# Kernel tuning notes

Measured on AMD Instinct MI355X. Metric: run time of the kernel, lower is better.

## Reference

```python
import jax, jax.numpy as jnp
import numpy as np

PAD_LABEL = 15
NUM_TAGS = 15


def setup_inputs() -> dict:
    key = jax.random.key(0)
    k1, k2, k3 = jax.random.split(key, 3)
    B, T, C = 4096, 512, NUM_TAGS
    logits = jax.random.normal(k1, (B, T, C), dtype=jnp.float32)
    y_true = jax.random.randint(k2, (B, T), 0, PAD_LABEL + 1, dtype=jnp.int32)
    # CRF transition matrix (learned param), glorot-ish scale
    transitions = jax.random.normal(k3, (C, C), dtype=jnp.float32) * 0.25
    return {"logits": logits, "y_true": y_true, "transitions": transitions}


def _log_norm(logits, transitions, mask):
    # logits: (B, T, C) float32, mask: (B, T) bool
    alpha0 = logits[:, 0, :]                       # (B, C)
    # scan over timesteps 1..T-1
    emits = jnp.swapaxes(logits[:, 1:, :], 0, 1)    # (T-1, B, C)
    masks = jnp.swapaxes(mask[:, 1:], 0, 1)         # (T-1, B)

    def step(alpha, inp):
        emit_t, mask_t = inp                        # (B, C), (B,)
        # scores[b, i, j] = alpha[b, i] + trans[i, j] + emit_t[b, j]
        scores = alpha[:, :, None] + transitions[None, :, :] + emit_t[:, None, :]
        new_alpha = jax.scipy.special.logsumexp(scores, axis=1)  # (B, C)
        alpha = jnp.where(mask_t[:, None], new_alpha, alpha)
        return alpha, None

    alpha, _ = jax.lax.scan(step, alpha0, (emits, masks))
    return jax.scipy.special.logsumexp(alpha, axis=1)  # (B,)


def _sequence_score(logits, transitions, labels, mask):
    mask_f = mask.astype(jnp.float32)
    safe_labels = jnp.where(mask, labels, 0)                    # (B, T)
    # emission scores along gold path
    em = jnp.take_along_axis(logits, safe_labels[:, :, None], axis=2)[:, :, 0]
    emission_score = jnp.sum(em * mask_f, axis=1)               # (B,)
    # transition scores between consecutive valid positions
    prev, curr = safe_labels[:, :-1], safe_labels[:, 1:]
    tmask_f = (mask[:, 1:] & mask[:, :-1]).astype(jnp.float32)
    trans_scores = transitions[prev, curr]                      # (B, T-1)
    transition_score = jnp.sum(trans_scores * tmask_f, axis=1)  # (B,)
    return emission_score + transition_score


def reference(logits, y_true, transitions):
    mask = y_true != PAD_LABEL                                  # (B, T) bool
    logZ = _log_norm(logits, transitions, mask)
    path_score = _sequence_score(logits, transitions, y_true, mask)
    nll = jnp.clip(logZ - path_score, 0.0, 1000000.0)
    return jnp.mean(nll)
```

## Files before the change

kernel.cpp:

```cpp
#include <hip/hip_runtime.h>
#include <hip/hip_bf16.h>

#define PAD 15
#define NTAGS 15
#define SEQ_T 512
#define SPB 8
#define LOG2E 1.4426950408889634f
#define LN2   0.6931471805599453f

__device__ __forceinline__ float max15(const float* A) {
  float m0 = fmaxf(fmaxf(A[0], A[1]), A[2]);
  float m1 = fmaxf(fmaxf(A[3], A[4]), A[5]);
  float m2 = fmaxf(fmaxf(A[6], A[7]), A[8]);
  float m3 = fmaxf(fmaxf(A[9], A[10]), A[11]);
  float m4 = fmaxf(fmaxf(A[12], A[13]), A[14]);
  return fmaxf(fmaxf(fmaxf(m0, m1), fmaxf(m2, m3)), m4);
}

__device__ __forceinline__ float dot15(const float* a, const float* b) {
  float d0 = a[0] * b[0], d1 = a[1] * b[1], d2 = a[2] * b[2];
  d0 = fmaf(a[3], b[3], d0);  d1 = fmaf(a[4], b[4], d1);  d2 = fmaf(a[5], b[5], d2);
  d0 = fmaf(a[6], b[6], d0);  d1 = fmaf(a[7], b[7], d1);  d2 = fmaf(a[8], b[8], d2);
  d0 = fmaf(a[9], b[9], d0);  d1 = fmaf(a[10], b[10], d1); d2 = fmaf(a[11], b[11], d2);
  d0 = fmaf(a[12], b[12], d0); d1 = fmaf(a[13], b[13], d1); d2 = fmaf(a[14], b[14], d2);
  return (d0 + d1) + d2;
}

__device__ __forceinline__ void bcast_read(const float4* slot4, float* E) {
  asm volatile("" ::: "memory");
  float4 u0 = slot4[0], u1 = slot4[1], u2 = slot4[2], u3 = slot4[3];
  E[0] = u0.x; E[1] = u0.y; E[2]  = u0.z; E[3]  = u0.w;
  E[4] = u1.x; E[5] = u1.y; E[6]  = u1.z; E[7]  = u1.w;
  E[8] = u2.x; E[9] = u2.y; E[10] = u2.z; E[11] = u2.w;
  E[12] = u3.x; E[13] = u3.y; E[14] = u3.z;
}

__global__ __launch_bounds__(256, 2)
void crf_fwdbwd(const float* __restrict__ logits, const int* __restrict__ yg,
                const float* __restrict__ trans, float* __restrict__ out)
{
  __shared__ float Tl[256];
  __shared__ int   yl[SPB * SEQ_T];
  __shared__ float bc[16][16];
  __shared__ float comb[SPB][32];
  __shared__ float blks[SPB];

  const int tid = threadIdx.x;

  Tl[tid] = (tid < NTAGS * NTAGS) ? trans[tid] : 0.0f;
  {
    const int4* src = (const int4*)(yg + (size_t)blockIdx.x * (SPB * SEQ_T));
    int4* dst = (int4*)yl;
    #pragma unroll
    for (int k = 0; k < (SPB * SEQ_T / 4) / 256; ++k)
      dst[tid + k * 256] = src[tid + k * 256];
  }
  __syncthreads();

  const int wave = tid >> 6;
  const int lane = tid & 63;
  const int j  = lane & 15;
  const int jj = (j < 15) ? j : 14;
  const int sLoc = (wave >> 1) * 4 + (lane >> 4);
  const bool isFwd = (wave & 1) == 0;
  const int seq = blockIdx.x * SPB + sLoc;
  float* slot = &bc[tid >> 4][0];
  const float4* slot4 = (const float4*)slot;
  const int* ys = &yl[sLoc * SEQ_T];
  const float* ebase = logits + (size_t)seq * (SEQ_T * NTAGS) + jj;

  float W[15];
  float pacc = 0.0f;

  if (isFwd) {
    #pragma unroll
    for (int i = 0; i < 15; ++i) W[i] = exp2f(Tl[i * 15 + jj] * LOG2E);

    float a0 = ebase[0];
    int yp = ys[0];
    pacc = (j == yp && yp != PAD) ? a0 : 0.0f;
    slot[j] = a0 * LOG2E;
    float A[15];
    bcast_read(slot4, A);
    float M = max15(A);
    float E[15];
    #pragma unroll
    for (int i = 0; i < 15; ++i) E[i] = exp2f(A[i] - M);
    float Eown = E[jj];

    float buf[8];
    #pragma unroll
    for (int k = 0; k < 8; ++k) buf[k] = ebase[(1 + k) * 15];

    for (int tb = 1; tb <= 241; tb += 8) {
      #pragma unroll
      for (int k = 0; k < 8; ++k) {
        const int t = tb + k;
        float emit = buf[k];
        int tn = t + 8; tn = (tn > 255) ? 255 : tn;
        buf[k] = ebase[tn * 15];
        int yc = ys[t];
        float p = exp2f(emit * LOG2E);
        float dot = dot15(E, W);
        float newE = dot * p;
        bool mk = (yc != PAD);
        float own = mk ? newE : Eown;
        float tv = Tl[yp * 15 + yc];
        float add = emit + ((yp != PAD) ? tv : 0.0f);
        pacc += (mk && (j == yc)) ? add : 0.0f;
        slot[j] = own;
        bcast_read(slot4, E);
        Eown = own;
        yp = yc;
        if (k == 7) {
          float m = max15(E);
          float rs = 1.0f / m;
          #pragma unroll
          for (int i = 0; i < 15; ++i) E[i] *= rs;
          Eown *= rs;
          M += log2f(m);
        }
      }
    }
    #pragma unroll
    for (int k = 0; k < 7; ++k) {
      const int t = 249 + k;
      float emit = buf[k];
      int yc = ys[t];
      float p = exp2f(emit * LOG2E);
      float dot = dot15(E, W);
      float newE = dot * p;
      bool mk = (yc != PAD);
      float own = mk ? newE : Eown;
      float tv = Tl[yp * 15 + yc];
      float add = emit + ((yp != PAD) ? tv : 0.0f);
      pacc += (mk && (j == yc)) ? add : 0.0f;
      slot[j] = own;
      bcast_read(slot4, E);
      Eown = own;
      yp = yc;
    }
    #pragma unroll
    for (int k = 1; k < 16; k <<= 1) pacc += __shfl_xor(pacc, k, 16);
    if (j < 15) comb[sLoc][j] = M + log2f(Eown);
    if (j == 0) comb[sLoc][30] = pacc;
  } else {
    #pragma unroll
    for (int i = 0; i < 15; ++i) W[i] = exp2f(Tl[jj * 15 + i] * LOG2E);

    float Eb = 1.0f, Mb = 0.0f;
    int yc = ys[511];
    float buf[8];
    #pragma unroll
    for (int k = 0; k < 8; ++k) buf[k] = ebase[(511 - k) * 15];

    float Q[15];
    for (int tb = 511; tb >= 271; tb -= 8) {
      #pragma unroll
      for (int k = 0; k < 8; ++k) {
        const int t = tb - k;
        float emit = buf[k];
        int tn = t - 8; tn = (tn < 256) ? 256 : tn;
        buf[k] = ebase[tn * 15];
        int yp2 = ys[t - 1];
        float p = exp2f(emit * LOG2E);
        float q = Eb * p;
        slot[j] = q;
        bcast_read(slot4, Q);
        float dot = dot15(W, Q);
        bool mk = (yc != PAD);
        Eb = mk ? dot : Eb;
        float tv = Tl[yp2 * 15 + yc];
        float add = emit + ((yp2 != PAD) ? tv : 0.0f);
        pacc += (mk && (j == yc)) ? add : 0.0f;
        yc = yp2;
        if (k == 7) {
          float m = max15(Q);
          float rs = 1.0f / m;
          Eb *= rs;
          Mb += log2f(m);
        }
      }
    }
    #pragma unroll
    for (int k = 0; k < 8; ++k) {
      const int t = 263 - k;
      float emit = buf[k];
      int yp2 = ys[t - 1];
      float p = exp2f(emit * LOG2E);
      float q = Eb * p;
      slot[j] = q;
      bcast_read(slot4, Q);
      float dot = dot15(W, Q);
      bool mk = (yc != PAD);
      Eb = mk ? dot : Eb;
      float tv = Tl[yp2 * 15 + yc];
      float add = emit + ((yp2 != PAD) ? tv : 0.0f);
      pacc += (mk && (j == yc)) ? add : 0.0f;
      yc = yp2;
    }
    #pragma unroll
    for (int k = 1; k < 16; k <<= 1) pacc += __shfl_xor(pacc, k, 16);
    if (j < 15) comb[sLoc][15 + j] = Mb + log2f(Eb);
    if (j == 0) comb[sLoc][31] = pacc;
  }

  __syncthreads();

  if (tid < SPB) {
    const float* c = comb[tid];
    float s[15];
    #pragma unroll
    for (int i = 0; i < 15; ++i) s[i] = c[i] + c[15 + i];
    float m = max15(s);
    float sum = 0.0f;
    #pragma unroll
    for (int i = 0; i < 15; ++i) sum += exp2f(s[i] - m);
    float logZ = (m + log2f(sum)) * LN2;
    float path = c[30] + c[31];
    float nll = logZ - path;
    nll = fminf(fmaxf(nll, 0.0f), 1000000.0f);
    blks[tid] = nll;
  }
  __syncthreads();
  if (tid == 0) {
    float tot = 0.0f;
    #pragma unroll
    for (int i = 0; i < SPB; ++i) tot += blks[i];
    atomicAdd(out, tot * (1.0f / 4096.0f));
  }
}

extern "C" void kernel_launch(void* const* d_in, const int* in_sizes, int n_in,
                              void* d_out, int out_size, void* d_ws, size_t ws_size,
                              hipStream_t stream) {
  const float* logits = (const float*)d_in[0];
  const int*   y      = (const int*)d_in[1];
  const float* trans  = (const float*)d_in[2];
  float* out = (float*)d_out;

  hipMemsetAsync(out, 0, sizeof(float), stream);

  const int B = in_sizes[1] / SEQ_T;
  const int blocks = B / SPB;
  crf_fwdbwd<<<dim3(blocks), dim3(256), 0, stream>>>(logits, y, trans, out);
}
```

Measured before the change: 66.48 us.

## Replace LDS broadcast with DPP gather and hoist gold-path scoring out of recursion

The per-step exchange of alpha values among the 16 lanes of a chain now uses DPP cross-lane moves (a butterfly gather of 16 values) instead of writing to and reading back from shared memory. The transition weights are permuted per lane to match the DPP gather order. The gold-path score is computed up front in a separate parallel pass over all 512 positions, so the recursive loop no longer handles it, and labels are streamed from global memory rather than staged in LDS. In exchange the loop does more cross-lane instructions per step and renormalises with a fast reciprocal, which adds a correctness risk around the edge lanes and the masking.

```diff
diff --git a/kernel.cpp b/kernel.cpp
--- a/kernel.cpp
+++ b/kernel.cpp
@@ -1,232 +1,188 @@
 #include <hip/hip_runtime.h>
-#include <hip/hip_bf16.h>
 
 #define PAD 15
-#define NTAGS 15
-#define SEQ_T 512
-#define SPB 8
 #define LOG2E 1.4426950408889634f
 #define LN2   0.6931471805599453f
 
-__device__ __forceinline__ float max15(const float* A) {
-  float m0 = fmaxf(fmaxf(A[0], A[1]), A[2]);
-  float m1 = fmaxf(fmaxf(A[3], A[4]), A[5]);
-  float m2 = fmaxf(fmaxf(A[6], A[7]), A[8]);
-  float m3 = fmaxf(fmaxf(A[9], A[10]), A[11]);
-  float m4 = fmaxf(fmaxf(A[12], A[13]), A[14]);
-  return fmaxf(fmaxf(fmaxf(m0, m1), fmaxf(m2, m3)), m4);
-}
-
-__device__ __forceinline__ float dot15(const float* a, const float* b) {
-  float d0 = a[0] * b[0], d1 = a[1] * b[1], d2 = a[2] * b[2];
-  d0 = fmaf(a[3], b[3], d0);  d1 = fmaf(a[4], b[4], d1);  d2 = fmaf(a[5], b[5], d2);
-  d0 = fmaf(a[6], b[6], d0);  d1 = fmaf(a[7], b[7], d1);  d2 = fmaf(a[8], b[8], d2);
-  d0 = fmaf(a[9], b[9], d0);  d1 = fmaf(a[10], b[10], d1); d2 = fmaf(a[11], b[11], d2);
-  d0 = fmaf(a[12], b[12], d0); d1 = fmaf(a[13], b[13], d1); d2 = fmaf(a[14], b[14], d2);
-  return (d0 + d1) + d2;
-}
-
-__device__ __forceinline__ void bcast_read(const float4* slot4, float* E) {
-  asm volatile("" ::: "memory");
-  float4 u0 = slot4[0], u1 = slot4[1], u2 = slot4[2], u3 = slot4[3];
-  E[0] = u0.x; E[1] = u0.y; E[2]  = u0.z; E[3]  = u0.w;
-  E[4] = u1.x; E[5] = u1.y; E[6]  = u1.z; E[7]  = u1.w;
-  E[8] = u2.x; E[9] = u2.y; E[10] = u2.z; E[11] = u2.w;
-  E[12] = u3.x; E[13] = u3.y; E[14] = u3.z;
+#define DPP_X1  0xB1
+#define DPP_X2  0x4E
+#define DPP_X7  0x141
+#define DPP_X15 0x140
+
+template<int CTRL>
+__device__ __forceinline__ float dppf(float x) {
+  int r = __builtin_amdgcn_update_dpp(0, __builtin_bit_cast(int, x), CTRL, 0xF, 0xF, true);
+  return __builtin_bit_cast(float, r);
+}
+
+__device__ __forceinline__ void gather16(float share, float* g) {
+  g[0] = share;
+  g[1] = dppf<DPP_X1>(g[0]);
+  g[2] = dppf<DPP_X2>(g[0]);  g[3] = dppf<DPP_X2>(g[1]);
+  g[4] = dppf<DPP_X7>(g[0]);  g[5] = dppf<DPP_X7>(g[1]);
+  g[6] = dppf<DPP_X7>(g[2]);  g[7] = dppf<DPP_X7>(g[3]);
+  g[8]  = dppf<DPP_X15>(g[0]); g[9]  = dppf<DPP_X15>(g[1]);
+  g[10] = dppf<DPP_X15>(g[2]); g[11] = dppf<DPP_X15>(g[3]);
+  g[12] = dppf<DPP_X15>(g[4]); g[13] = dppf<DPP_X15>(g[5]);
+  g[14] = dppf<DPP_X15>(g[6]); g[15] = dppf<DPP_X15>(g[7]);
+}
+
+__device__ __forceinline__ float max16(const float* g) {
+  float a = fmaxf(g[0], g[1]),  b = fmaxf(g[2], g[3]);
+  float c = fmaxf(g[4], g[5]),  d = fmaxf(g[6], g[7]);
+  float e = fmaxf(g[8], g[9]),  f = fmaxf(g[10], g[11]);
+  float h = fmaxf(g[12], g[13]), i = fmaxf(g[14], g[15]);
+  return fmaxf(fmaxf(fmaxf(a, b), fmaxf(c, d)), fmaxf(fmaxf(e, f), fmaxf(h, i)));
+}
+
+__device__ __forceinline__ float dot16(const float* g, const float* W) {
+  float d0 = g[0] * W[0], d1 = g[1] * W[1], d2 = g[2] * W[2], d3 = g[3] * W[3];
+  d0 = fmaf(g[4],  W[4],  d0); d1 = fmaf(g[5],  W[5],  d1);
+  d2 = fmaf(g[6],  W[6],  d2); d3 = fmaf(g[7],  W[7],  d3);
+  d0 = fmaf(g[8],  W[8],  d0); d1 = fmaf(g[9],  W[9],  d1);
+  d2 = fmaf(g[10], W[10], d2); d3 = fmaf(g[11], W[11], d3);
+  d0 = fmaf(g[12], W[12], d0); d1 = fmaf(g[13], W[13], d1);
+  d2 = fmaf(g[14], W[14], d2); d3 = fmaf(g[15], W[15], d3);
+  return (d0 + d1) + (d2 + d3);
+}
+
+template<bool RN>
+__device__ __forceinline__ void crf_step(float emit, int yv, bool isBwd,
+                                         const float* Wg, float& own, float& M) {
+  const float p = exp2f(emit * LOG2E);
+  const float share = own * (isBwd ? p : 1.0f);
+  float g[16];
+  gather16(share, g);
+  const float tot = dot16(g, Wg);
+  const float cand = tot * (isBwd ? 1.0f : p);
+  own = (yv != PAD) ? cand : own;
+  if (RN) {
+    const float m = max16(g);
+    const float rs = __builtin_amdgcn_rcpf(m);
+    own *= rs;
+    M += log2f(m);
+  }
 }
 
 __global__ __launch_bounds__(256, 2)
-void crf_fwdbwd(const float* __restrict__ logits, const int* __restrict__ yg,
-                const float* __restrict__ trans, float* __restrict__ out)
-{
-  __shared__ float Tl[256];
-  __shared__ int   yl[SPB * SEQ_T];
-  __shared__ float bc[16][16];
-  __shared__ float comb[SPB][32];
-  __shared__ float blks[SPB];
+void crf_kernel(const float* __restrict__ logits, const int* __restrict__ yg,
+                const float* __restrict__ trans, float* __restrict__ out) {
+  __shared__ float Tl[240];
+  __shared__ float comb[8][2][16];
+  __shared__ float path8[8];
+  __shared__ float blks[8];
 
   const int tid = threadIdx.x;
-
-  Tl[tid] = (tid < NTAGS * NTAGS) ? trans[tid] : 0.0f;
+  if (tid < 225) Tl[tid] = trans[tid];
+  __syncthreads();
+
+  const char* lb = (const char*)logits;
+  const char* yb = (const char*)yg;
+
   {
-    const int4* src = (const int4*)(yg + (size_t)blockIdx.x * (SPB * SEQ_T));
-    int4* dst = (int4*)yl;
-    #pragma unroll
-    for (int k = 0; k < (SPB * SEQ_T / 4) / 256; ++k)
-      dst[tid + k * 256] = src[tid + k * 256];
-  }
-  __syncthreads();
-
-  const int wave = tid >> 6;
-  const int lane = tid & 63;
-  const int j  = lane & 15;
-  const int jj = (j < 15) ? j : 14;
-  const int sLoc = (wave >> 1) * 4 + (lane >> 4);
-  const bool isFwd = (wave & 1) == 0;
-  const int seq = blockIdx.x * SPB + sLoc;
-  float* slot = &bc[tid >> 4][0];
-  const float4* slot4 = (const float4*)slot;
-  const int* ys = &yl[sLoc * SEQ_T];
-  const float* ebase = logits + (size_t)seq * (SEQ_T * NTAGS) + jj;
-
-  float W[15];
-  float pacc = 0.0f;
-
-  if (isFwd) {
-    #pragma unroll
-    for (int i = 0; i < 15; ++i) W[i] = exp2f(Tl[i * 15 + jj] * LOG2E);
-
-    float a0 = ebase[0];
-    int yp = ys[0];
-    pacc = (j == yp && yp != PAD) ? a0 : 0.0f;
-    slot[j] = a0 * LOG2E;
-    float A[15];
-    bcast_read(slot4, A);
-    float M = max15(A);
-    float E[15];
-    #pragma unroll
-    for (int i = 0; i < 15; ++i) E[i] = exp2f(A[i] - M);
-    float Eown = E[jj];
-
-    float buf[8];
-    #pragma unroll
-    for (int k = 0; k < 8; ++k) buf[k] = ebase[(1 + k) * 15];
-
-    for (int tb = 1; tb <= 241; tb += 8) {
-      #pragma unroll
-      for (int k = 0; k < 8; ++k) {
-        const int t = tb + k;
-        float emit = buf[k];
-        int tn = t + 8; tn = (tn > 255) ? 255 : tn;
-        buf[k] = ebase[tn * 15];
-        int yc = ys[t];
-        float p = exp2f(emit * LOG2E);
-        float dot = dot15(E, W);
-        float newE = dot * p;
-        bool mk = (yc != PAD);
-        float own = mk ? newE : Eown;
-        float tv = Tl[yp * 15 + yc];
-        float add = emit + ((yp != PAD) ? tv : 0.0f);
-        pacc += (mk && (j == yc)) ? add : 0.0f;
-        slot[j] = own;
-        bcast_read(slot4, E);
-        Eown = own;
-        yp = yc;
-        if (k == 7) {
-          float m = max15(E);
-          float rs = 1.0f / m;
-          #pragma unroll
-          for (int i = 0; i < 15; ++i) E[i] *= rs;
-          Eown *= rs;
-          M += log2f(m);
+    const int q = tid >> 5;
+    const int l32 = tid & 31;
+    const int ps = blockIdx.x * 8 + q;
+    const int ybase = ps * 2048;
+    const int ebase = ps * 30720;
+    float acc = 0.0f;
+    #pragma unroll
+    for (int m = 0; m < 16; ++m) {
+      const int t = l32 + 32 * m;
+      const int yc = *(const int*)(yb + ybase + t * 4);
+      if (yc != PAD) {
+        acc += *(const float*)(lb + ebase + t * 60 + yc * 4);
+        if (t > 0) {
+          const int yp = *(const int*)(yb + ybase + t * 4 - 4);
+          if (yp != PAD) acc += Tl[yp * 15 + yc];
         }
       }
     }
     #pragma unroll
-    for (int k = 0; k < 7; ++k) {
-      const int t = 249 + k;
-      float emit = buf[k];
-      int yc = ys[t];
-      float p = exp2f(emit * LOG2E);
-      float dot = dot15(E, W);
-      float newE = dot * p;
-      bool mk = (yc != PAD);
-      float own = mk ? newE : Eown;
-      float tv = Tl[yp * 15 + yc];
-      float add = emit + ((yp != PAD) ? tv : 0.0f);
-      pacc += (mk && (j == yc)) ? add : 0.0f;
-      slot[j] = own;
-      bcast_read(slot4, E);
-      Eown = own;
-      yp = yc;
+    for (int k = 1; k < 32; k <<= 1) acc += __shfl_xor(acc, k, 32);
+    if (l32 == 0) path8[q] = acc;
+  }
+
+  const int lane = tid & 63;
+  const int wave = tid >> 6;
+  const int row  = lane >> 4;
+  const int j    = lane & 15;
+  const int jj   = (j < 15) ? j : 14;
+  const int chain = wave * 4 + row;
+  const int sloc  = chain >> 1;
+  const bool isBwd = (chain & 1) != 0;
+  const int seq = blockIdx.x * 8 + sloc;
+
+  constexpr int xm[16] = {0, 1, 2, 3, 7, 6, 5, 4, 15, 14, 13, 12, 8, 9, 10, 11};
+  float Wg[16];
+  #pragma unroll
+  for (int r = 0; r < 16; ++r) {
+    const int src = j ^ xm[r];
+    const bool valid = (j < 15) && (src < 15);
+    const int ti = valid ? (isBwd ? j * 15 + src : src * 15 + j) : 0;
+    Wg[r] = valid ? exp2f(Tl[ti] * LOG2E) : 0.0f;
+  }
+
+  int eoff = seq * 30720 + (isBwd ? 511 * 60 : 0) + jj * 4;
+  int yoff = seq * 2048 + (isBwd ? 511 * 4 : 0);
+  const int de = isBwd ? -60 : 60;
+  const int dy = isBwd ? -4 : 4;
+
+  float buf[8]; int ybuf[8];
+  #pragma unroll
+  for (int i = 0; i < 8; ++i) {
+    buf[i]  = *(const float*)(lb + (eoff + i * de));
+    ybuf[i] = *(const int*)(yb + (yoff + i * dy));
+  }
+  int peoff = eoff + 8 * de;
+  int pyoff = yoff + 8 * dy;
+
+  const float a0 = buf[0];
+  const float A = (j < 15) ? a0 * LOG2E : -1.0e30f;
+  float gi[16];
+  gather16(A, gi);
+  const float Mf = max16(gi);
+  float own = isBwd ? ((j < 15) ? 1.0f : 0.0f) : exp2f(A - Mf);
+  float M   = isBwd ? 0.0f : Mf;
+  if (!isBwd) ybuf[0] = PAD;
+
+  for (int sb = 0; sb < 32; ++sb) {
+    #pragma unroll
+    for (int kk = 0; kk < 8; ++kk) {
+      const float emit = buf[kk];
+      const int yv = ybuf[kk];
+      buf[kk]  = *(const float*)(lb + peoff);
+      ybuf[kk] = *(const int*)(yb + pyoff);
+      peoff += de; pyoff += dy;
+      if (kk == 7) crf_step<true>(emit, yv, isBwd, Wg, own, M);
+      else         crf_step<false>(emit, yv, isBwd, Wg, own, M);
     }
-    #pragma unroll
-    for (int k = 1; k < 16; k <<= 1) pacc += __shfl_xor(pacc, k, 16);
-    if (j < 15) comb[sLoc][j] = M + log2f(Eown);
-    if (j == 0) comb[sLoc][30] = pacc;
-  } else {
-    #pragma unroll
-    for (int i = 0; i < 15; ++i) W[i] = exp2f(Tl[jj * 15 + i] * LOG2E);
-
-    float Eb = 1.0f, Mb = 0.0f;
-    int yc = ys[511];
-    float buf[8];
-    #pragma unroll
-    for (int k = 0; k < 8; ++k) buf[k] = ebase[(511 - k) * 15];
-
-    float Q[15];
-    for (int tb = 511; tb >= 271; tb -= 8) {
-      #pragma unroll
-      for (int k = 0; k < 8; ++k) {
-        const int t = tb - k;
-        float emit = buf[k];
-        int tn = t - 8; tn = (tn < 256) ? 256 : tn;
-        buf[k] = ebase[tn * 15];
-        int yp2 = ys[t - 1];
-        float p = exp2f(emit * LOG2E);
-        float q = Eb * p;
-        slot[j] = q;
-        bcast_read(slot4, Q);
-        float dot = dot15(W, Q);
-        bool mk = (yc != PAD);
-        Eb = mk ? dot : Eb;
-        float tv = Tl[yp2 * 15 + yc];
-        float add = emit + ((yp2 != PAD) ? tv : 0.0f);
-        pacc += (mk && (j == yc)) ? add : 0.0f;
-        yc = yp2;
-        if (k == 7) {
-          float m = max15(Q);
-          float rs = 1.0f / m;
-          Eb *= rs;
-          Mb += log2f(m);
-        }
-      }
+  }
+
+  const float logv = (j < 15 && own > 0.0f) ? (M + log2f(own)) : -1.0e30f;
+  comb[sloc][isBwd ? 1 : 0][j] = logv;
+  __syncthreads();
+
+  if (tid < 8) {
+    float sv[15];
+    float mx = -3.0e38f;
+    #pragma unroll
+    for (int i = 0; i < 15; ++i) {
+      sv[i] = comb[tid][0][i] + comb[tid][1][i];
+      mx = fmaxf(mx, sv[i]);
     }
-    #pragma unroll
-    for (int k = 0; k < 8; ++k) {
-      const int t = 263 - k;
-      float emit = buf[k];
-      int yp2 = ys[t - 1];
-      float p = exp2f(emit * LOG2E);
-      float q = Eb * p;
-      slot[j] = q;
-      bcast_read(slot4, Q);
-      float dot = dot15(W, Q);
-      bool mk = (yc != PAD);
-      Eb = mk ? dot : Eb;
-      float tv = Tl[yp2 * 15 + yc];
-      float add = emit + ((yp2 != PAD) ? tv : 0.0f);
-      pacc += (mk && (j == yc)) ? add : 0.0f;
-      yc = yp2;
-    }
-    #pragma unroll
-    for (int k = 1; k < 16; k <<= 1) pacc += __shfl_xor(pacc, k, 16);
-    if (j < 15) comb[sLoc][15 + j] = Mb + log2f(Eb);
-    if (j == 0) comb[sLoc][31] = pacc;
-  }
-
-  __syncthreads();
-
-  if (tid < SPB) {
-    const float* c = comb[tid];
-    float s[15];
-    #pragma unroll
-    for (int i = 0; i < 15; ++i) s[i] = c[i] + c[15 + i];
-    float m = max15(s);
-    float sum = 0.0f;
-    #pragma unroll
-    for (int i = 0; i < 15; ++i) sum += exp2f(s[i] - m);
-    float logZ = (m + log2f(sum)) * LN2;
-    float path = c[30] + c[31];
-    float nll = logZ - path;
+    float vs = 0.0f;
+    #pragma unroll
+    for (int i = 0; i < 15; ++i) vs += exp2f(sv[i] - mx);
+    const float logZ = (mx + log2f(vs)) * LN2;
+    float nll = logZ - path8[tid];
     nll = fminf(fmaxf(nll, 0.0f), 1000000.0f);
     blks[tid] = nll;
   }
   __syncthreads();
   if (tid == 0) {
-    float tot = 0.0f;
-    #pragma unroll
-    for (int i = 0; i < SPB; ++i) tot += blks[i];
+    float tot = (blks[0] + blks[1]) + (blks[2] + blks[3]) +
+                (blks[4] + blks[5]) + (blks[6] + blks[7]);
     atomicAdd(out, tot * (1.0f / 4096.0f));
   }
 }
@@ -241,7 +197,6 @@
 
   hipMemsetAsync(out, 0, sizeof(float), stream);
 
-  const int B = in_sizes[1] / SEQ_T;
-  const int blocks = B / SPB;
-  crf_fwdbwd<<<dim3(blocks), dim3(256), 0, stream>>>(logits, y, trans, out);
-}
+  const int B = in_sizes[1] / 512;
+  crf_kernel<<<dim3(B / 8), dim3(256), 0, stream>>>(logits, y, trans, out);
+}
```

After: 79.12 us. +19.0%, slower.
